# Kernel optimization log

Measured on AMD Instinct MI355X. Metric: run time of the kernel, lower is better.

Reference implementation:

```python
import jax, jax.numpy as jnp
import numpy as np

BSZ, N, E, D = 8, 1024, 49152, 256
K, ALPHA = 10, 0.1
EDGE_RATIO, NODE_RATIO = 0.8, 0.7
K_NODES = int(np.ceil(NODE_RATIO * N))  # torch_geometric topk uses ceil -> 717


def setup_inputs() -> dict:
    key = jax.random.key(0)
    ks = jax.random.split(key, 10)
    concept_hidden = jax.random.normal(ks[0], (BSZ, N, D), jnp.float32)
    head = jax.random.randint(ks[1], (BSZ, E), 0, N, jnp.int32)
    off = jax.random.randint(ks[2], (BSZ, E), 1, N, jnp.int32)
    tail = ((head + off) % N).astype(jnp.int32)  # guaranteed no self-loops
    triple_label = jnp.ones((BSZ, E), jnp.int32)  # all edges valid (no -1 padding)
    relation_hidden = jnp.zeros((BSZ, 1), jnp.float32)  # unused by the math
    concept_labels = jax.random.randint(ks[3], (BSZ, N), 0, 3, jnp.int32)
    concept_ids = jax.random.randint(ks[4], (BSZ, N), 0, 50000, jnp.int32)
    # PageRank temp (learnable param, deterministic init from alpha/K)
    t = ALPHA * (1.0 - ALPHA) ** np.arange(K + 1)
    t[-1] = (1.0 - ALPHA) ** K
    temp = jnp.asarray(t, jnp.float32)
    # GraphAttention params (heads=1)
    g = float(np.sqrt(6.0 / (D + D)))
    W_proj = jax.random.uniform(ks[5], (D, D), jnp.float32, -g, g)
    ga = float(np.sqrt(6.0 / (1 + D)))
    a_src = jax.random.uniform(ks[6], (D,), jnp.float32, -ga, ga)
    a_tgt = jax.random.uniform(ks[7], (D,), jnp.float32, -ga, ga)
    # output Linear(2D -> D)
    gl = float(np.sqrt(1.0 / (2 * D)))
    W_lin = jax.random.uniform(ks[8], (D, 2 * D), jnp.float32, -gl, gl)
    b_lin = jax.random.uniform(ks[9], (D,), jnp.float32, -gl, gl)
    return dict(concept_hidden=concept_hidden, relation_hidden=relation_hidden,
                head=head, tail=tail, triple_label=triple_label,
                concept_labels=concept_labels, concept_ids=concept_ids,
                temp=temp, W_proj=W_proj, a_src=a_src, a_tgt=a_tgt,
                W_lin=W_lin, b_lin=b_lin)


def _per_sample(x, h, t, labels, ids, temp, W_proj, a_src, a_tgt, W_lin, b_lin):
    # ---- PageRank (gcn_norm with added self-loops, aggr='add' into tail) ----
    sl = jnp.arange(N, dtype=jnp.int32)
    hs = jnp.concatenate([h, sl])
    ts = jnp.concatenate([t, sl])
    deg = jax.ops.segment_sum(jnp.ones(E + N, x.dtype), ts, num_segments=N)
    dinv = jnp.where(deg > 0, jax.lax.rsqrt(deg), 0.0)
    norm = dinv[hs] * dinv[ts]  # [E+N]

    def step(xk, gamma):
        xk = jax.ops.segment_sum(norm[:, None] * xk[hs], ts, num_segments=N)
        return xk, gamma * xk

    _, contribs = jax.lax.scan(step, x, temp[1:])  # K steps
    x_cut = temp[0] * x + contribs.sum(0)  # [N, D]

    # ---- edge attention (GAT-style scoring, sigmoid) ----
    proj = x_cut @ W_proj.T                       # [N, D] (heads=1)
    s_src = proj @ a_src                          # [N]
    s_tgt = proj @ a_tgt                          # [N]
    attn = jax.nn.sigmoid(s_src[h] + s_tgt[t])    # [E]

    # ---- symmetrize + coalesce(mean), done densely ----
    rows = jnp.concatenate([h, t])
    cols = jnp.concatenate([t, h])
    vals = jnp.concatenate([attn, attn])
    S = jnp.zeros((N, N), x.dtype).at[rows, cols].add(vals)
    Cn = jnp.zeros((N, N), x.dtype).at[rows, cols].add(1.0)
    valid = Cn > 0
    A = jnp.where(valid, S / jnp.maximum(Cn, 1.0), 0.0)  # coalesced mean adjacency

    # ---- np.percentile(attn, 20) with linear interpolation over valid edges ----
    sv = jnp.sort(jnp.where(valid, A, jnp.inf).reshape(-1))  # valid values first
    M = valid.sum()
    pos = (1.0 - EDGE_RATIO) * (M.astype(x.dtype) - 1.0)
    lo = jnp.floor(pos).astype(jnp.int32)
    frac = pos - lo.astype(x.dtype)
    hi = jnp.minimum(lo + 1, M - 1)  # stays within the finite (valid) prefix
    cut = sv[lo] + frac * (sv[hi] - sv[lo])

    A_cut = jnp.where(valid & (A >= cut), A, 0.0)  # edges below percentile zeroed

    # ---- node scoring: scatter_add of attn*x[src] into dst == A_cut^T @ x ----
    out = A_cut.T @ x                              # [N, D]
    score = jnp.abs(out).sum(1) + 1e-7             # [N]
    _, perm = jax.lax.top_k(score, K_NODES)

    pooled = A_cut[perm] @ x                       # [k, D]
    hcat = jnp.concatenate([x[perm], pooled], axis=-1)  # [k, 2D]
    h_new = hcat @ W_lin.T + b_lin                 # [k, D]
    return h_new, labels[perm], ids[perm]


def reference(concept_hidden, relation_hidden, head, tail, triple_label,
              concept_labels, concept_ids, temp, W_proj, a_src, a_tgt,
              W_lin, b_lin):
    f = jax.vmap(_per_sample,
                 in_axes=(0, 0, 0, 0, 0, None, None, None, None, None, None))
    return f(concept_hidden, head, tail, concept_labels, concept_ids,
             temp, W_proj, a_src, a_tgt, W_lin, b_lin)
```

## Files before the change

kernel.cpp:

```cpp
#include <hip/hip_runtime.h>
#include <math.h>

#define BSZ 8
#define NN 1024
#define EE 49152
#define DD 256
#define KSTEPS 10
#define NCH 192
#define KNODES 717
#define RS 256
#define MROWS 720
#define SELB 64

typedef __attribute__((ext_vector_type(8))) short short8_t;
typedef __attribute__((ext_vector_type(4))) float f32x4;

__device__ __forceinline__ void fma4(float4& a, float w, const float4 v) {
    a.x += w * v.x; a.y += w * v.y; a.z += w * v.z; a.w += w * v.w;
}

__device__ __forceinline__ unsigned short f2bf(float f) {
    unsigned u = __float_as_uint(f);
    u = (u + 0x7fffu + ((u >> 16) & 1u)) >> 16;
    return (unsigned short)u;
}


__global__ void k_hist(const int* __restrict__ head, const int* __restrict__ tail,
                       int* __restrict__ cnt_t, int* __restrict__ cnt_h,
                       const float* __restrict__ Wl, unsigned short* __restrict__ Wb) {
    __shared__ int lt[NN];
    __shared__ int lh[NN];
    int tid = threadIdx.x;
    if (blockIdx.x >= BSZ * NCH) {
        int i = (blockIdx.x - BSZ * NCH) * 256 + tid;
        Wb[i] = f2bf(Wl[i]);
        return;
    }
    int b = blockIdx.x / NCH, ch = blockIdx.x % NCH;
    for (int i = tid; i < NN; i += 256) { lt[i] = 0; lh[i] = 0; }
    __syncthreads();
    int e = ch * 256 + tid;
    int h = head[b * EE + e], t = tail[b * EE + e];
    atomicAdd(&lt[t], 1);
    atomicAdd(&lh[h], 1);
    __syncthreads();
    int base = (b * NCH + ch) * NN;
    for (int i = tid; i < NN; i += 256) { cnt_t[base + i] = lt[i]; cnt_h[base + i] = lh[i]; }
}

__global__ void k_chunkscan(int* __restrict__ cnt_t, int* __restrict__ cnt_h,
                            int* __restrict__ tot_t, int* __restrict__ tot_h,
                            float* __restrict__ dinv) {
    int gid = blockIdx.x * 256 + threadIdx.x;
    int which = gid >> 13;
    int i = gid & 8191;
    int b = i >> 10, n = i & 1023;
    int* c = which ? cnt_h : cnt_t;
    int run = 0;
    for (int s = 0; s < NCH; s++) {
        int idx = (b * NCH + s) * NN + n;
        int v = c[idx];
        c[idx] = run;
        run += v;
    }
    (which ? tot_h : tot_t)[i] = run;
    if (!which) dinv[i] = 1.0f / sqrtf((float)(run + 1));
}

__global__ __launch_bounds__(1024) void k_nodescan(const int* __restrict__ tot_t,
                                                   const int* __restrict__ tot_h,
                                                   int* __restrict__ toff, int* __restrict__ hoff) {
    __shared__ int sb[NN];
    int b = blockIdx.x >> 1, which = blockIdx.x & 1;
    int tid = threadIdx.x;
    const int* tot = which ? tot_h : tot_t;
    int* off = which ? hoff : toff;
    int v = tot[b * NN + tid];
    sb[tid] = v;
    __syncthreads();
    for (int o = 1; o < NN; o <<= 1) {
        int t = (tid >= o) ? sb[tid - o] : 0;
        __syncthreads();
        sb[tid] += t;
        __syncthreads();
    }
    off[b * (NN + 1) + tid] = sb[tid] - v;
    if (tid == NN - 1) off[b * (NN + 1) + NN] = sb[tid];
}

__global__ void k_fill(const int* __restrict__ head, const int* __restrict__ tail,
                       const int* __restrict__ cnt_t, const int* __restrict__ cnt_h,
                       const int* __restrict__ toff, const int* __restrict__ hoff,
                       const float* __restrict__ dinv,
                       int* __restrict__ t_head, float* __restrict__ t_norm,
                       int* __restrict__ h_tail) {
    __shared__ int sh[256], st[256];
    int b = blockIdx.x / NCH, ch = blockIdx.x % NCH;
    int tid = threadIdx.x;
    int e = ch * 256 + tid;
    int h = head[b * EE + e], t = tail[b * EE + e];
    sh[tid] = h;
    st[tid] = t;
    __syncthreads();
    int rt = 0, rh = 0;
    for (int j = 0; j < tid; j++) {
        rt += (st[j] == t);
        rh += (sh[j] == h);
    }
    int post = toff[b * (NN + 1) + t] + cnt_t[(b * NCH + ch) * NN + t] + rt;
    t_head[b * EE + post] = h;
    t_norm[b * EE + post] = dinv[b * NN + h] * dinv[b * NN + t];
    int posh = hoff[b * (NN + 1) + h] + cnt_h[(b * NCH + ch) * NN + h] + rh;
    h_tail[b * EE + posh] = t;
}

__global__ __launch_bounds__(256) void k_prstep(const float* __restrict__ src, float* __restrict__ dst,
                         float* __restrict__ xacc, const float* __restrict__ temp,
                         const int* __restrict__ toff, const int* __restrict__ t_head,
                         const float* __restrict__ t_norm, const float* __restrict__ dinv,
                         int kidx,
                         const float* __restrict__ Wp, const float* __restrict__ as_,
                         const float* __restrict__ at_, float* __restrict__ vsrc,
                         float* __restrict__ vtgt) {
    if (blockIdx.x >= BSZ * NN / 4) {
        int d = threadIdx.x;
        float vs = 0.f, vt = 0.f;
        for (int i = 0; i < DD; i++) {
            float w = Wp[i * DD + d];
            vs += as_[i] * w;
            vt += at_[i] * w;
        }
        vsrc[d] = vs;
        vtgt[d] = vt;
        return;
    }
    int wid = threadIdx.x >> 6, lane = threadIdx.x & 63;
    int b = blockIdx.x & 7;
    int n = (blockIdx.x >> 3) * 4 + wid;
    int g = b * NN + n;
    int o0 = __builtin_amdgcn_readfirstlane(toff[b * (NN + 1) + n]);
    int o1 = __builtin_amdgcn_readfirstlane(toff[b * (NN + 1) + n + 1]);
    int ebase = __builtin_amdgcn_readfirstlane(b * EE);
    const int* __restrict__ hp = t_head + ebase;
    const float* __restrict__ wp = t_norm + ebase;
    float dv = dinv[g];
    const float4* src4 = (const float4*)src;
    size_t r4 = (size_t)g * 64 + lane;
    size_t bb = (size_t)b * NN * 64;
    float4 sv = src4[r4];
    float sl = dv * dv;
    float4 acc;
    acc.x = sl * sv.x; acc.y = sl * sv.y; acc.z = sl * sv.z; acc.w = sl * sv.w;
    int j = o0;
    for (; j + 8 <= o1; j += 8) {
        int c0 = hp[j], c1 = hp[j + 1], c2 = hp[j + 2], c3 = hp[j + 3];
        int c4 = hp[j + 4], c5 = hp[j + 5], c6 = hp[j + 6], c7 = hp[j + 7];
        float w0 = wp[j], w1 = wp[j + 1], w2 = wp[j + 2], w3 = wp[j + 3];
        float w4 = wp[j + 4], w5 = wp[j + 5], w6 = wp[j + 6], w7 = wp[j + 7];
        float4 xa = src4[bb + (size_t)c0 * 64 + lane];
        float4 xb = src4[bb + (size_t)c1 * 64 + lane];
        float4 xc = src4[bb + (size_t)c2 * 64 + lane];
        float4 xd = src4[bb + (size_t)c3 * 64 + lane];
        float4 xe = src4[bb + (size_t)c4 * 64 + lane];
        float4 xf = src4[bb + (size_t)c5 * 64 + lane];
        float4 xg = src4[bb + (size_t)c6 * 64 + lane];
        float4 xh = src4[bb + (size_t)c7 * 64 + lane];
        fma4(acc, w0, xa); fma4(acc, w1, xb); fma4(acc, w2, xc); fma4(acc, w3, xd);
        fma4(acc, w4, xe); fma4(acc, w5, xf); fma4(acc, w6, xg); fma4(acc, w7, xh);
    }
    for (; j + 4 <= o1; j += 4) {
        int c0 = hp[j], c1 = hp[j + 1], c2 = hp[j + 2], c3 = hp[j + 3];
        float w0 = wp[j], w1 = wp[j + 1], w2 = wp[j + 2], w3 = wp[j + 3];
        float4 xa = src4[bb + (size_t)c0 * 64 + lane];
        float4 xb = src4[bb + (size_t)c1 * 64 + lane];
        float4 xc = src4[bb + (size_t)c2 * 64 + lane];
        float4 xd = src4[bb + (size_t)c3 * 64 + lane];
        fma4(acc, w0, xa); fma4(acc, w1, xb); fma4(acc, w2, xc); fma4(acc, w3, xd);
    }
    for (; j < o1; j++) {
        int c0 = hp[j];
        float w0 = wp[j];
        float4 xa = src4[bb + (size_t)c0 * 64 + lane];
        fma4(acc, w0, xa);
    }
    ((float4*)dst)[r4] = acc;
    float gm = temp[kidx + 1];
    float4 xa2;
    if (kidx == 0) {
        float t0 = temp[0];
        xa2.x = t0 * sv.x; xa2.y = t0 * sv.y; xa2.z = t0 * sv.z; xa2.w = t0 * sv.w;
    } else {
        xa2 = ((float4*)xacc)[r4];
    }
    fma4(xa2, gm, acc);
    ((float4*)xacc)[r4] = xa2;
}


__global__ void k_s(const float* __restrict__ xacc, const float* __restrict__ vsrc,
                    const float* __restrict__ vtgt, float* __restrict__ ssrc,
                    float* __restrict__ stgt) {
    int g = blockIdx.x * 4 + (threadIdx.x >> 6);
    int lane = threadIdx.x & 63;
    const float4* xr = (const float4*)(xacc + (size_t)g * DD);
    float4 xv = xr[lane];
    float4 vs = ((const float4*)vsrc)[lane];
    float4 vt = ((const float4*)vtgt)[lane];
    float s1 = xv.x * vs.x + xv.y * vs.y + xv.z * vs.z + xv.w * vs.w;
    float s2 = xv.x * vt.x + xv.y * vt.y + xv.z * vt.z + xv.w * vt.w;
    for (int o = 32; o > 0; o >>= 1) {
        s1 += __shfl_down(s1, o);
        s2 += __shfl_down(s2, o);
    }
    if (lane == 0) {
        ssrc[g] = s1;
        stgt[g] = s2;
    }
}


__global__ __launch_bounds__(256) void k_rowbuild(const int* __restrict__ hoff, const int* __restrict__ h_tail,
                          const int* __restrict__ toff, const int* __restrict__ t_head,
                          const float* __restrict__ ssrc, const float* __restrict__ stgt,
                          int* __restrict__ rcol, float* __restrict__ rval,
                          int* __restrict__ nnzrow) {
    __shared__ int cols[RS];
    __shared__ float vals[RS];
    __shared__ int first[NN];
    __shared__ int cntb[NN];
    __shared__ unsigned pres[32];
    int g = blockIdx.x;
    int b = g >> 10, n = g & 1023;
    int tid = threadIdx.x;
    int a0 = hoff[b * (NN + 1) + n], a1 = hoff[b * (NN + 1) + n + 1];
    int c0 = toff[b * (NN + 1) + n], c1 = toff[b * (NN + 1) + n + 1];
    int kh = a1 - a0;
    int kk = kh + (c1 - c0);
    if (kk > RS) kk = RS;
    ((int4*)first)[tid] = make_int4(0x7fffffff, 0x7fffffff, 0x7fffffff, 0x7fffffff);
    ((int4*)cntb)[tid] = make_int4(0, 0, 0, 0);
    if (tid < 32) pres[tid] = 0;
    float sn = ssrc[g], tn = stgt[g];
    __syncthreads();
    if (tid < kk) {
        int c;
        float z;
        if (tid < kh) { c = h_tail[b * EE + a0 + tid]; z = sn + stgt[b * NN + c]; }
        else          { c = t_head[b * EE + c0 + (tid - kh)]; z = ssrc[b * NN + c] + tn; }
        cols[tid] = c;
        vals[tid] = 1.0f / (1.0f + expf(-z));
        atomicMin(&first[c], tid);
        atomicAdd(&cntb[c], 1);
        atomicOr(&pres[c >> 5], 1u << (c & 31));
    }
    __syncthreads();
    if (tid == 0) {
        int tot = 0;
        for (int w = 0; w < 32; w++) tot += __popc(pres[w]);
        nnzrow[g] = tot;
    }
    if (tid < kk) {
        int c = cols[tid];
        if (first[c] == tid) {
            int cc = cntb[c];
            float v;
            if (cc == 1) {
                v = vals[tid];
            } else {
                float s = 0.f;
                for (int j = tid; j < kk; j++)
                    if (cols[j] == c) s += vals[j];
                v = s / (float)cc;
            }
            int w = c >> 5;
            int r = __popc(pres[w] & ((1u << (c & 31)) - 1u));
            for (int u = 0; u < w; u++) r += __popc(pres[u]);
            size_t rb = ((size_t)g << 8) + r;
            rcol[rb] = c;
            rval[rb] = v;
        }
    }
}


__global__ void k_selinit(const int* __restrict__ nnzrow, int* __restrict__ sel) {
    __shared__ int red[256];
    int b = blockIdx.x, tid = threadIdx.x;
    int s = nnzrow[b * NN + tid] + nnzrow[b * NN + 256 + tid] +
            nnzrow[b * NN + 512 + tid] + nnzrow[b * NN + 768 + tid];
    red[tid] = s;
    __syncthreads();
    for (int o = 128; o > 0; o >>= 1) {
        if (tid < o) red[tid] += red[tid + o];
        __syncthreads();
    }
    if (tid == 0) {
        int M = red[0];
        float pos = 0.2f * ((float)M - 1.0f);
        int lo = (int)floorf(pos);
        float frac = pos - (float)lo;
        sel[b * 8 + 0] = lo;
        sel[b * 8 + 1] = min(lo + 1, M - 1);
        sel[b * 8 + 2] = 0;
        sel[b * 8 + 3] = 0;
        sel[b * 8 + 4] = __float_as_int(frac);
    }
}

__global__ void k_selhist(const float* __restrict__ rval, const int* __restrict__ nnzrow,
                          const int* __restrict__ sel, int* __restrict__ hist, int pass) {
    __shared__ int lh[512];
    int tid = threadIdx.x;
    lh[tid] = 0;
    lh[tid + 256] = 0;
    __syncthreads();
    int b = blockIdx.x / SELB, blk = blockIdx.x % SELB;
    unsigned p0 = (unsigned)sel[b * 8 + 2];
    unsigned p1 = (unsigned)sel[b * 8 + 3];
    int shift = 24 - 8 * pass;
    for (int r = 0; r < NN / SELB; r++) {
        int g = b * NN + blk * (NN / SELB) + r;
        int nnz = nnzrow[g];
        const float* vp = rval + ((size_t)g << 8);
        for (int i = tid; i < nnz; i += 256) {
            unsigned bits = __float_as_uint(vp[i]);
            unsigned bucket = (bits >> shift) & 255u;
            if (pass == 0) {
                atomicAdd(&lh[bucket], 1);
                atomicAdd(&lh[256 + bucket], 1);
            } else {
                unsigned hb = bits >> (shift + 8);
                if (hb == p0) atomicAdd(&lh[bucket], 1);
                if (hb == p1) atomicAdd(&lh[256 + bucket], 1);
            }
        }
    }
    __syncthreads();
    int v0 = lh[tid];
    if (v0) atomicAdd(&hist[(b * 2 + 0) * 256 + tid], v0);
    int v1 = lh[tid + 256];
    if (v1) atomicAdd(&hist[(b * 2 + 1) * 256 + tid], v1);
}

__global__ void k_selreduce(int* __restrict__ hist, int* __restrict__ sel) {
    __shared__ int sb[256];
    int b = blockIdx.x >> 1, ch = blockIdx.x & 1;
    int tid = threadIdx.x;
    int idx = (b * 2 + ch) * 256 + tid;
    int v = hist[idx];
    hist[idx] = 0;
    int rem = sel[b * 8 + ch];
    int pref = sel[b * 8 + 2 + ch];
    sb[tid] = v;
    __syncthreads();
    for (int o = 1; o < 256; o <<= 1) {
        int t = (tid >= o) ? sb[tid - o] : 0;
        __syncthreads();
        sb[tid] += t;
        __syncthreads();
    }
    int excl = sb[tid] - v;
    if (v > 0 && rem >= excl && rem < excl + v) {
        sel[b * 8 + ch] = rem - excl;
        sel[b * 8 + 2 + ch] = (pref << 8) | tid;
    }
}

__global__ void k_cut(const int* __restrict__ sel, float* __restrict__ cut) {
    int b = threadIdx.x;
    if (b < BSZ) {
        float v0 = __uint_as_float((unsigned)sel[b * 8 + 2]);
        float v1 = __uint_as_float((unsigned)sel[b * 8 + 3]);
        float frac = __int_as_float(sel[b * 8 + 4]);
        cut[b] = v0 + frac * (v1 - v0);
    }
}


__global__ __launch_bounds__(256) void k_outscore(const int* __restrict__ rcol, const float* __restrict__ rval,
                           const int* __restrict__ nnzrow, const float* __restrict__ x,
                           const float* __restrict__ cut, float* __restrict__ out_pr,
                           float* __restrict__ score) {
    int wid = threadIdx.x >> 6, lane = threadIdx.x & 63;
    int b = blockIdx.x & 7;
    int n = (blockIdx.x >> 3) * 4 + wid;
    int g = b * NN + n;
    float cb = cut[b];
    int nnz = __builtin_amdgcn_readfirstlane(nnzrow[g]);
    int rbase = __builtin_amdgcn_readfirstlane(g << 8);
    const int* __restrict__ cp = rcol + rbase;
    const float* __restrict__ vp = rval + rbase;
    const float4* x4 = (const float4*)x;
    size_t bb = (size_t)b * NN * 64;
    float4 acc = make_float4(0.f, 0.f, 0.f, 0.f);
    int j = 0;
    for (; j + 4 <= nnz; j += 4) {
        float a0 = vp[j], a1 = vp[j + 1], a2 = vp[j + 2], a3 = vp[j + 3];
        int c0 = cp[j], c1 = cp[j + 1], c2 = cp[j + 2], c3 = cp[j + 3];
        float4 xa = x4[bb + (size_t)c0 * 64 + lane];
        float4 xb = x4[bb + (size_t)c1 * 64 + lane];
        float4 xc = x4[bb + (size_t)c2 * 64 + lane];
        float4 xd = x4[bb + (size_t)c3 * 64 + lane];
        if (a0 >= cb) fma4(acc, a0, xa);
        if (a1 >= cb) fma4(acc, a1, xb);
        if (a2 >= cb) fma4(acc, a2, xc);
        if (a3 >= cb) fma4(acc, a3, xd);
    }
    for (; j < nnz; j++) {
        float a0 = vp[j];
        int c0 = cp[j];
        float4 xa = x4[bb + (size_t)c0 * 64 + lane];
        if (a0 >= cb) fma4(acc, a0, xa);
    }
    ((float4*)out_pr)[(size_t)g * 64 + lane] = acc;
    float4 r;
    r.x = fabsf(acc.x); r.y = fabsf(acc.y); r.z = fabsf(acc.z); r.w = fabsf(acc.w);
    for (int o = 32; o > 0; o >>= 1) {
        r.x += __shfl_down(r.x, o);
        r.y += __shfl_down(r.y, o);
        r.z += __shfl_down(r.z, o);
        r.w += __shfl_down(r.w, o);
    }
    r.x += r.z;
    r.y += r.w;
    r.x += r.y;
    if (lane == 0) score[g] = r.x + 1e-7f;
}


__global__ __launch_bounds__(1024) void k_topk(const float* __restrict__ score,
                                               const int* __restrict__ labels,
                                               const int* __restrict__ ids,
                                               int* __restrict__ perm,
                                               float* __restrict__ out_lab,
                                               float* __restrict__ out_ids) {
    __shared__ float sc[NN];
    __shared__ int idx[NN];
    int b = blockIdx.x, tid = threadIdx.x;
    sc[tid] = score[b * NN + tid];
    idx[tid] = tid;
    __syncthreads();
    for (int k = 2; k <= NN; k <<= 1) {
        for (int j = k >> 1; j > 0; j >>= 1) {
            int p = tid ^ j;
            if (p > tid) {
                float s0 = sc[tid], s1 = sc[p];
                int i0 = idx[tid], i1 = idx[p];
                bool before01 = (s0 > s1) || (s0 == s1 && i0 < i1);
                bool up = ((tid & k) == 0);
                bool sw = up ? (!before01) : before01;
                if (sw) {
                    sc[tid] = s1; sc[p] = s0;
                    idx[tid] = i1; idx[p] = i0;
                }
            }
            __syncthreads();
        }
    }
    perm[b * NN + tid] = idx[tid];
    if (tid < KNODES) {
        int p = idx[tid];
        out_lab[b * KNODES + tid] = (float)labels[b * NN + p];
        out_ids[b * KNODES + tid] = (float)ids[b * NN + p];
    }
}


__global__ void k_packA(const float* __restrict__ x, const float* __restrict__ outpr,
                        const int* __restrict__ perm, unsigned short* __restrict__ A16) {
    int row = blockIdx.x;
    int b = row / MROWS, i = row - b * MROWS;
    int tid = threadIdx.x;
    size_t ob = (size_t)row * 512;
    if (i < KNODES) {
        int p = perm[b * NN + i];
        float v0 = x[((size_t)(b * NN + p)) * DD + tid];
        float v1 = outpr[((size_t)(b * NN + p)) * DD + tid];
        A16[ob + tid] = f2bf(v0);
        A16[ob + 256 + tid] = f2bf(v1);
    } else {
        A16[ob + tid] = 0;
        A16[ob + 256 + tid] = 0;
    }
}

__global__ __launch_bounds__(256) void k_hnew_mfma(const unsigned short* __restrict__ A16,
                                                   const unsigned short* __restrict__ Wb,
                                                   const float* __restrict__ b_lin,
                                                   float* __restrict__ hnew) {
    int w = blockIdx.x * 4 + (threadIdx.x >> 6);
    int lane = threadIdx.x & 63;
    int b = w / (45 * 16);
    int rem = w - b * (45 * 16);
    int mt = rem >> 4, nt = rem & 15;
    int m = lane & 15, quad = lane >> 4;
    const unsigned short* ap = A16 + ((size_t)(b * MROWS + mt * 16 + m) * 512 + quad * 8);
    const unsigned short* bp = Wb + ((size_t)(nt * 16 + m) * 512 + quad * 8);
    f32x4 acc = {0.f, 0.f, 0.f, 0.f};
#pragma unroll
    for (int s = 0; s < 16; s++) {
        short8_t av = *(const short8_t*)(ap + s * 32);
        short8_t bv = *(const short8_t*)(bp + s * 32);
        acc = __builtin_amdgcn_mfma_f32_16x16x32_bf16(av, bv, acc, 0, 0, 0);
    }
    int d = nt * 16 + m;
    float bl = b_lin[d];
#pragma unroll
    for (int r = 0; r < 4; r++) {
        int i = mt * 16 + quad * 4 + r;
        if (i < KNODES) hnew[((size_t)(b * KNODES + i)) * DD + d] = acc[r] + bl;
    }
}


extern "C" void kernel_launch(void* const* d_in, const int* in_sizes, int n_in,
                              void* d_out, int out_size, void* d_ws, size_t ws_size,
                              hipStream_t stream) {
    const float* x      = (const float*)d_in[0];
    const int*   head   = (const int*)d_in[2];
    const int*   tail   = (const int*)d_in[3];
    const int*   labels = (const int*)d_in[5];
    const int*   ids    = (const int*)d_in[6];
    const float* temp   = (const float*)d_in[7];
    const float* Wp     = (const float*)d_in[8];
    const float* asrc   = (const float*)d_in[9];
    const float* atgt   = (const float*)d_in[10];
    const float* Wl     = (const float*)d_in[11];
    const float* blin   = (const float*)d_in[12];

    float* out_h   = (float*)d_out;
    float* out_lab = out_h + (size_t)BSZ * KNODES * DD;
    float* out_ids = out_lab + (size_t)BSZ * KNODES;

    size_t o = 0;
    char* ws = (char*)d_ws;
    auto A_ = [&](size_t bytes) -> void* {
        void* p = ws + o;
        o += (bytes + 255) & ~(size_t)255;
        return p;
    };
    int*   cnt_t  = (int*)  A_((size_t)BSZ * NCH * NN * 4);
    int*   cnt_h  = (int*)  A_((size_t)BSZ * NCH * NN * 4);
    int*   tot_t  = (int*)  A_((size_t)BSZ * NN * 4);
    int*   tot_h  = (int*)  A_((size_t)BSZ * NN * 4);
    int*   toff   = (int*)  A_((size_t)BSZ * (NN + 1) * 4);
    int*   hoff   = (int*)  A_((size_t)BSZ * (NN + 1) * 4);
    float* dinv   = (float*)A_((size_t)BSZ * NN * 4);
    int*   t_head = (int*)  A_((size_t)BSZ * EE * 4);
    float* t_norm = (float*)A_((size_t)BSZ * EE * 4);
    int*   h_tail = (int*)  A_((size_t)BSZ * EE * 4);
    float* xkA    = (float*)A_((size_t)BSZ * NN * DD * 4);
    float* xkB    = (float*)A_((size_t)BSZ * NN * DD * 4);
    float* xacc   = (float*)A_((size_t)BSZ * NN * DD * 4);
    float* vsrc   = (float*)A_(DD * 4);
    float* vtgt   = (float*)A_(DD * 4);
    float* ssrc   = (float*)A_((size_t)BSZ * NN * 4);
    float* stgt   = (float*)A_((size_t)BSZ * NN * 4);
    int*   rcol   = (int*)  A_((size_t)BSZ * NN * RS * 4);
    float* rval   = (float*)A_((size_t)BSZ * NN * RS * 4);
    int*   nnzrow = (int*)  A_((size_t)BSZ * NN * 4);
    int*   sel    = (int*)  A_(BSZ * 8 * 4);
    int*   hist   = (int*)  A_(BSZ * 2 * 256 * 4);
    float* cutv   = (float*)A_(BSZ * 4);
    float* outpr  = (float*)A_((size_t)BSZ * NN * DD * 4);
    float* scorev = (float*)A_((size_t)BSZ * NN * 4);
    int*   perm   = (int*)  A_((size_t)BSZ * NN * 4);
    unsigned short* Wb16 = (unsigned short*)A_((size_t)DD * 512 * 2);
    unsigned short* A16  = (unsigned short*)A_((size_t)BSZ * MROWS * 512 * 2);
    if (o > ws_size) return;

    hipMemsetAsync(hist, 0, BSZ * 2 * 256 * 4, stream);

    k_hist<<<BSZ * NCH + 512, 256, 0, stream>>>(head, tail, cnt_t, cnt_h, Wl, Wb16);
    k_chunkscan<<<64, 256, 0, stream>>>(cnt_t, cnt_h, tot_t, tot_h, dinv);
    k_nodescan<<<16, 1024, 0, stream>>>(tot_t, tot_h, toff, hoff);
    k_fill<<<BSZ * NCH, 256, 0, stream>>>(head, tail, cnt_t, cnt_h, toff, hoff, dinv,
                                          t_head, t_norm, h_tail);
    for (int k = 0; k < KSTEPS; k++) {
        const float* src = (k == 0) ? x : ((k & 1) ? xkA : xkB);
        float* dst = (k & 1) ? xkB : xkA;
        int grid = BSZ * NN / 4 + ((k == KSTEPS - 1) ? 1 : 0);
        k_prstep<<<grid, 256, 0, stream>>>(src, dst, xacc, temp, toff, t_head, t_norm, dinv, k,
                                           Wp, asrc, atgt, vsrc, vtgt);
    }
    k_s<<<BSZ * NN / 4, 256, 0, stream>>>(xacc, vsrc, vtgt, ssrc, stgt);
    k_rowbuild<<<BSZ * NN, 256, 0, stream>>>(hoff, h_tail, toff, t_head, ssrc, stgt,
                                             rcol, rval, nnzrow);
    k_selinit<<<BSZ, 256, 0, stream>>>(nnzrow, sel);
    for (int p = 0; p < 4; p++) {
        k_selhist<<<BSZ * SELB, 256, 0, stream>>>(rval, nnzrow, sel, hist, p);
        k_selreduce<<<16, 256, 0, stream>>>(hist, sel);
    }
    k_cut<<<1, 64, 0, stream>>>(sel, cutv);
    k_outscore<<<BSZ * NN / 4, 256, 0, stream>>>(rcol, rval, nnzrow, x, cutv, outpr, scorev);
    k_topk<<<BSZ, 1024, 0, stream>>>(scorev, labels, ids, perm, out_lab, out_ids);
    k_packA<<<BSZ * MROWS, 256, 0, stream>>>(x, outpr, perm, A16);
    k_hnew_mfma<<<BSZ * 45 * 16 / 4, 256, 0, stream>>>(A16, Wb16, blin, out_h);
}
```

Before: 443.6 us.

## Spread chunk scan over more blocks, privatize selection histograms, bound PageRank occupancy

The chunk scan now runs as 256 blocks of 64 threads instead of 64 blocks of 256, and its serial loop is unrolled by four so more loads are in flight and more CUs are busy. The selection histogram keeps four sub-histograms per block, chosen by thread index, which cuts shared-memory atomic contention. In pass 0 it also drops the duplicate atomic and reuses the same count for both outputs. The PageRank step gets a minimum-occupancy launch bound, which may cap registers and risk spills.

```diff
diff --git a/kernel.cpp b/kernel.cpp
--- a/kernel.cpp
+++ b/kernel.cpp
@@ -49,20 +49,23 @@
     for (int i = tid; i < NN; i += 256) { cnt_t[base + i] = lt[i]; cnt_h[base + i] = lh[i]; }
 }
 
-__global__ void k_chunkscan(int* __restrict__ cnt_t, int* __restrict__ cnt_h,
+__global__ __launch_bounds__(64) void k_chunkscan(int* __restrict__ cnt_t, int* __restrict__ cnt_h,
                             int* __restrict__ tot_t, int* __restrict__ tot_h,
                             float* __restrict__ dinv) {
-    int gid = blockIdx.x * 256 + threadIdx.x;
+    int gid = blockIdx.x * 64 + threadIdx.x;
     int which = gid >> 13;
     int i = gid & 8191;
     int b = i >> 10, n = i & 1023;
     int* c = which ? cnt_h : cnt_t;
+    int base = b * NCH * NN + n;
     int run = 0;
-    for (int s = 0; s < NCH; s++) {
-        int idx = (b * NCH + s) * NN + n;
-        int v = c[idx];
-        c[idx] = run;
-        run += v;
+    for (int s = 0; s < NCH; s += 4) {
+        int i0 = base + s * NN, i1 = i0 + NN, i2 = i1 + NN, i3 = i2 + NN;
+        int v0 = c[i0], v1 = c[i1], v2 = c[i2], v3 = c[i3];
+        c[i0] = run; run += v0;
+        c[i1] = run; run += v1;
+        c[i2] = run; run += v2;
+        c[i3] = run; run += v3;
     }
     (which ? tot_h : tot_t)[i] = run;
     if (!which) dinv[i] = 1.0f / sqrtf((float)(run + 1));
@@ -115,7 +118,7 @@
     h_tail[b * EE + posh] = t;
 }
 
-__global__ __launch_bounds__(256) void k_prstep(const float* __restrict__ src, float* __restrict__ dst,
+__global__ __launch_bounds__(256, 6) void k_prstep(const float* __restrict__ src, float* __restrict__ dst,
                          float* __restrict__ xacc, const float* __restrict__ temp,
                          const int* __restrict__ toff, const int* __restrict__ t_head,
                          const float* __restrict__ t_norm, const float* __restrict__ dinv,
@@ -310,15 +313,16 @@
 
 __global__ void k_selhist(const float* __restrict__ rval, const int* __restrict__ nnzrow,
                           const int* __restrict__ sel, int* __restrict__ hist, int pass) {
-    __shared__ int lh[512];
+    __shared__ int lh0[1024];
+    __shared__ int lh1[1024];
     int tid = threadIdx.x;
-    lh[tid] = 0;
-    lh[tid + 256] = 0;
+    for (int u = tid; u < 1024; u += 256) { lh0[u] = 0; lh1[u] = 0; }
     __syncthreads();
     int b = blockIdx.x / SELB, blk = blockIdx.x % SELB;
     unsigned p0 = (unsigned)sel[b * 8 + 2];
     unsigned p1 = (unsigned)sel[b * 8 + 3];
     int shift = 24 - 8 * pass;
+    int sub = (tid & 3) << 8;
     for (int r = 0; r < NN / SELB; r++) {
         int g = b * NN + blk * (NN / SELB) + r;
         int nnz = nnzrow[g];
@@ -327,19 +331,18 @@
             unsigned bits = __float_as_uint(vp[i]);
             unsigned bucket = (bits >> shift) & 255u;
             if (pass == 0) {
-                atomicAdd(&lh[bucket], 1);
-                atomicAdd(&lh[256 + bucket], 1);
+                atomicAdd(&lh0[sub + bucket], 1);
             } else {
                 unsigned hb = bits >> (shift + 8);
-                if (hb == p0) atomicAdd(&lh[bucket], 1);
-                if (hb == p1) atomicAdd(&lh[256 + bucket], 1);
+                if (hb == p0) atomicAdd(&lh0[sub + bucket], 1);
+                if (hb == p1) atomicAdd(&lh1[sub + bucket], 1);
             }
         }
     }
     __syncthreads();
-    int v0 = lh[tid];
+    int v0 = lh0[tid] + lh0[256 + tid] + lh0[512 + tid] + lh0[768 + tid];
+    int v1 = (pass == 0) ? v0 : (lh1[tid] + lh1[256 + tid] + lh1[512 + tid] + lh1[768 + tid]);
     if (v0) atomicAdd(&hist[(b * 2 + 0) * 256 + tid], v0);
-    int v1 = lh[tid + 256];
     if (v1) atomicAdd(&hist[(b * 2 + 1) * 256 + tid], v1);
 }
 
@@ -573,7 +576,7 @@
     hipMemsetAsync(hist, 0, BSZ * 2 * 256 * 4, stream);
 
     k_hist<<<BSZ * NCH + 512, 256, 0, stream>>>(head, tail, cnt_t, cnt_h, Wl, Wb16);
-    k_chunkscan<<<64, 256, 0, stream>>>(cnt_t, cnt_h, tot_t, tot_h, dinv);
+    k_chunkscan<<<256, 64, 0, stream>>>(cnt_t, cnt_h, tot_t, tot_h, dinv);
     k_nodescan<<<16, 1024, 0, stream>>>(tot_t, tot_h, toff, hoff);
     k_fill<<<BSZ * NCH, 256, 0, stream>>>(head, tail, cnt_t, cnt_h, toff, hoff, dinv,
                                           t_head, t_norm, h_tail);
```

Result: no change. 441.5 us (-0.5%).
